# Performance work log

Measured on AMD Instinct MI355X. Metric: run time of the kernel, lower is better.

The kernel has to match this reference:

```python
import jax, jax.numpy as jnp
import numpy as np
import math

# irreps_in1 = 256x0e + 128x1e (dim 640); irreps_in2 = 1x0e + 1x1e (dim 4)
# TP/gate-input irreps = 256x0e + 128x0e + 128x1e (dim 768)
# gate output irreps   = 256x0e + 128x1e (dim 640)
MUL_S, MUL_V = 256, 128
DIM_IN1, DIM_IN2 = MUL_S + 3 * MUL_V, 4
FAN_IN = DIM_IN1 * DIM_IN2
N = 100000

# e3nn normalize2mom constants: 1/sqrt(E[f(x)^2]), x~N(0,1), via Gauss-Hermite
def _second_moment(f):
    t, w = np.polynomial.hermite.hermgauss(200)
    x = np.sqrt(2.0) * t
    return float(np.sum(w * f(x) ** 2) / np.sqrt(np.pi))

SILU_C = 1.0 / math.sqrt(_second_moment(lambda x: x / (1.0 + np.exp(-x))))
SIG_C = 1.0 / math.sqrt(_second_moment(lambda x: 1.0 / (1.0 + np.exp(-x))))

# e3nn path coefficients: sqrt(dim(ir_out) * path_weight / sum_paths_into_out) * w3j scale
# sum_paths (uvw, element norm) = sum(mul1*mul2) over instructions with same i_out
_XS01 = 256 + 128   # paths into each scalar output block
_XS2 = 256 + 128 + 128  # paths into vector output block
C0 = math.sqrt(1 * (256 * 256 * 1) / _XS01)                   # 0e x 0e -> 256x0e
C1 = math.sqrt(1 * (256 * 128 * 1) / _XS01) / math.sqrt(3.0)  # 1e x 1e -> 256x0e
C2 = math.sqrt(1 * (128 * 256 * 1) / _XS01)                   # 0e x 0e -> 128x0e
C3 = math.sqrt(1 * (128 * 128 * 1) / _XS01) / math.sqrt(3.0)  # 1e x 1e -> 128x0e
C4 = math.sqrt(3 * (128 * 256 * 1) / _XS2) / math.sqrt(3.0)   # 0e x 1e -> 128x1e
C5 = math.sqrt(3 * (128 * 128 * 1) / _XS2) / math.sqrt(3.0)   # 1e x 0e -> 128x1e
C6 = math.sqrt(3 * (128 * 128 * 1) / _XS2) / math.sqrt(6.0)   # 1e x 1e -> 128x1e (cross)


def setup_inputs() -> dict:
    key = jax.random.key(0)
    ks = jax.random.split(key, 10)
    return {
        'x': jax.random.normal(ks[0], (N, DIM_IN1), jnp.float32),
        'y': jax.random.normal(ks[1], (N, DIM_IN2), jnp.float32),
        'W0': jax.random.normal(ks[2], (256, 256), jnp.float32),
        'W1': jax.random.normal(ks[3], (128, 256), jnp.float32),
        'W2': jax.random.normal(ks[4], (256, 128), jnp.float32),
        'W3': jax.random.normal(ks[5], (128, 128), jnp.float32),
        'W4': jax.random.normal(ks[6], (256, 128), jnp.float32),
        'W5': jax.random.normal(ks[7], (128, 128), jnp.float32),
        'W6': jax.random.normal(ks[8], (128, 128), jnp.float32),
        'b': jax.random.normal(ks[9], (384,), jnp.float32) * 0.02,
    }


def reference(x, y, W0, W1, W2, W3, W4, W5, W6, b):
    n = x.shape[0]
    x0 = x[:, :MUL_S]                               # [N,256] scalars
    x1 = x[:, MUL_S:].reshape(n, MUL_V, 3)          # [N,128,3] vectors
    y0 = y[:, 0]                                    # [N]
    y1 = y[:, 1:]                                   # [N,3]

    x0y0 = x0 * y0[:, None]                         # [N,256]
    dot = jnp.einsum('zui,zi->zu', x1, y1)          # [N,128] (1e x 1e -> 0e)

    s1 = C0 * (x0y0 @ W0) + C1 * (dot @ W1)         # [N,256] scalar block
    s2 = C2 * (x0y0 @ W2) + C3 * (dot @ W3)         # [N,128] gate block

    va = C4 * (x0 @ W4)[:, :, None] * y1[:, None, :]            # 0e x 1e -> 1e
    vb = C5 * jnp.einsum('zui,uw->zwi', x1, W5) * y0[:, None, None]  # 1e x 0e -> 1e
    cross = jnp.cross(x1, y1[:, None, :])                        # [N,128,3]
    vc = C6 * jnp.einsum('zui,uw->zwi', cross, W6)               # 1e x 1e -> 1e
    v = va + vb + vc                                 # [N,128,3]

    inv = 1.0 / math.sqrt(FAN_IN)                    # rescale by sqrt(fan_in)
    s1 = s1 * inv + b[:MUL_S]
    s2 = s2 * inv + b[MUL_S:]
    v = v * inv

    out_s = SILU_C * jax.nn.silu(s1)                 # [N,256]
    gates = SIG_C * jax.nn.sigmoid(s2)               # [N,128]
    out_v = v * gates[:, :, None]                    # [N,128,3]
    return jnp.concatenate([out_s, out_v.reshape(n, -1)], axis=1)  # [N,640]
```

## Files before the change

kernel.cpp:

```cpp
#include <hip/hip_runtime.h>
#include <cmath>


typedef __bf16 bf16_t;
typedef bf16_t bf16x8 __attribute__((ext_vector_type(8)));
typedef bf16_t bf16x4 __attribute__((ext_vector_type(4)));
typedef float  f32x4  __attribute__((ext_vector_type(4)));

#define BM 32
#define KP 768

#define WU0 0
#define WD1 65536
#define WU2 98304
#define WD3 131072
#define WU4 147456
#define WR  180224
#define WQ  196608
#define WTOT 212992

#define MFMA(acc, av, bv) acc = __builtin_amdgcn_mfma_f32_16x16x32_bf16(av, bv, acc, 0, 0, 0)

__global__ void prep_weights(const float* __restrict__ W0, const float* __restrict__ W1,
                             const float* __restrict__ W2, const float* __restrict__ W3,
                             const float* __restrict__ W4, const float* __restrict__ W5,
                             const float* __restrict__ W6, bf16_t* __restrict__ WT,
                             float c0, float c1, float c2, float c3,
                             float c4, float c5, float c6)
{
    int idx = blockIdx.x * 256 + threadIdx.x;
    if (idx >= WTOT) return;
    float v;
    if (idx < WD1)      { int c = idx >> 8, k = idx & 255;                    v = c0 * W0[k * 256 + c]; }
    else if (idx < WU2) { int j = idx - WD1; int c = j >> 7, k = j & 127;     v = c1 * W1[k * 256 + c]; }
    else if (idx < WD3) { int j = idx - WU2; int c = j >> 8, k = j & 255;     v = c2 * W2[k * 128 + c]; }
    else if (idx < WU4) { int j = idx - WD3; int c = j >> 7, k = j & 127;     v = c3 * W3[k * 128 + c]; }
    else if (idx < WR)  { int j = idx - WU4; int c = j >> 8, k = j & 255;     v = c4 * W4[k * 128 + c]; }
    else if (idx < WQ)  { int j = idx - WR;  int c = j >> 7, k = j & 127;     v = c5 * W5[k * 128 + c]; }
    else                { int j = idx - WQ;  int c = j >> 7, k = j & 127;     v = c6 * W6[k * 128 + c]; }
    WT[idx] = (bf16_t)v;
}

__global__ __launch_bounds__(512) void tp_fused(
    const float* __restrict__ x, const float* __restrict__ y,
    const float* __restrict__ bias, const bf16_t* __restrict__ WT,
    float* __restrict__ out, float inv, float silu_c, float sig_c)
{
    __shared__ __attribute__((aligned(16))) bf16_t A[BM * KP];
    __shared__ float ylds[BM][4];

    const int tid = threadIdx.x;
    const int l   = tid & 63;
    const int w   = tid >> 6;
    const int l15 = l & 15;
    const int lg  = l >> 4;
    const int z0  = blockIdx.x * BM;

    if (tid < BM * 4) ylds[tid >> 2][tid & 3] = y[z0 * 4 + tid];

    #pragma unroll
    for (int it = 0; it < 4; ++it) {
        int f4 = tid + it * 512;
        int r = f4 >> 6, c4 = f4 & 63;
        float4 xv = *(const float4*)(x + (z0 + r) * 640 + c4 * 4);
        bf16x4 o;
        o[0] = (bf16_t)xv.x; o[1] = (bf16_t)xv.y; o[2] = (bf16_t)xv.z; o[3] = (bf16_t)xv.w;
        *(bf16x4*)&A[r * KP + ((c4 * 4) ^ ((r & 7) << 3))] = o;
    }
    #pragma unroll
    for (int it = 0; it < 8; ++it) {
        int e = tid + it * 512;
        int r = e >> 7, u = e & 127;
        const float* xp = x + (z0 + r) * 640 + 256 + u * 3;
        float a0 = xp[0], a1 = xp[1], a2 = xp[2];
        float4 yv = *(const float4*)(y + (z0 + r) * 4);
        int sw = (r & 7) << 3, base = r * KP;
        A[base + ((256 + u) ^ sw)] = (bf16_t)(a0 * yv.y + a1 * yv.z + a2 * yv.w);
        A[base + ((384 + u) ^ sw)] = (bf16_t)a0;
        A[base + ((512 + u) ^ sw)] = (bf16_t)a1;
        A[base + ((640 + u) ^ sw)] = (bf16_t)a2;
    }
    __syncthreads();

    const int asw    = (l15 & 7) << 3;
    const int a0base = l15 * KP;
    const int a1base = (16 + l15) * KP;
    const int klane  = lg * 8;

    {
        f32x4 sU[2][2], sD[2][2];
        #pragma unroll
        for (int a = 0; a < 2; ++a)
            #pragma unroll
            for (int b = 0; b < 2; ++b) { f32x4 z = {0.f,0.f,0.f,0.f}; sU[a][b] = z; sD[a][b] = z; }

        const bf16_t* b0p = WT + WU0 + ((w    ) * 16 + l15) * 256 + klane;
        const bf16_t* b1p = WT + WU0 + ((w + 8) * 16 + l15) * 256 + klane;
        const bf16_t* d0p = WT + WD1 + ((w    ) * 16 + l15) * 128 + klane;
        const bf16_t* d1p = WT + WD1 + ((w + 8) * 16 + l15) * 128 + klane;

        #pragma unroll
        for (int kk = 0; kk < 8; ++kk) {
            bf16x8 a0 = *(const bf16x8*)&A[a0base + ((kk * 32 + klane) ^ asw)];
            bf16x8 a1 = *(const bf16x8*)&A[a1base + ((kk * 32 + klane) ^ asw)];
            bf16x8 bb = *(const bf16x8*)(b0p + kk * 32);
            MFMA(sU[0][0], a0, bb); MFMA(sU[0][1], a1, bb);
            bb = *(const bf16x8*)(b1p + kk * 32);
            MFMA(sU[1][0], a0, bb); MFMA(sU[1][1], a1, bb);
        }
        #pragma unroll
        for (int kk = 0; kk < 4; ++kk) {
            bf16x8 a0 = *(const bf16x8*)&A[a0base + ((256 + kk * 32 + klane) ^ asw)];
            bf16x8 a1 = *(const bf16x8*)&A[a1base + ((256 + kk * 32 + klane) ^ asw)];
            bf16x8 bb = *(const bf16x8*)(d0p + kk * 32);
            MFMA(sD[0][0], a0, bb); MFMA(sD[0][1], a1, bb);
            bb = *(const bf16x8*)(d1p + kk * 32);
            MFMA(sD[1][0], a0, bb); MFMA(sD[1][1], a1, bb);
        }
        #pragma unroll
        for (int cs = 0; cs < 2; ++cs) {
            int col = (w + 8 * cs) * 16 + l15;
            float bv = bias[col];
            #pragma unroll
            for (int rt = 0; rt < 2; ++rt)
                #pragma unroll
                for (int rg = 0; rg < 4; ++rg) {
                    int lr = rt * 16 + lg * 4 + rg;
                    float sv = (ylds[lr][0] * sU[cs][rt][rg] + sD[cs][rt][rg]) * inv + bv;
                    out[(z0 + lr) * 640 + col] = silu_c * sv / (1.0f + __expf(-sv));
                }
        }
    }

    {
        f32x4 vU2[2], vU4[2], vD3[2], vR[3][2], vQ[3][2];
        #pragma unroll
        for (int rt = 0; rt < 2; ++rt) {
            f32x4 z = {0.f,0.f,0.f,0.f};
            vU2[rt] = z; vU4[rt] = z; vD3[rt] = z;
            #pragma unroll
            for (int i = 0; i < 3; ++i) { vR[i][rt] = z; vQ[i][rt] = z; }
        }
        const bf16_t* pu2 = WT + WU2 + (w * 16 + l15) * 256 + klane;
        const bf16_t* pu4 = WT + WU4 + (w * 16 + l15) * 256 + klane;
        const bf16_t* pd3 = WT + WD3 + (w * 16 + l15) * 128 + klane;
        const bf16_t* pr  = WT + WR  + (w * 16 + l15) * 128 + klane;
        const bf16_t* pq  = WT + WQ  + (w * 16 + l15) * 128 + klane;

        #pragma unroll
        for (int kk = 0; kk < 8; ++kk) {
            bf16x8 a0 = *(const bf16x8*)&A[a0base + ((kk * 32 + klane) ^ asw)];
            bf16x8 a1 = *(const bf16x8*)&A[a1base + ((kk * 32 + klane) ^ asw)];
            bf16x8 bb = *(const bf16x8*)(pu2 + kk * 32);
            MFMA(vU2[0], a0, bb); MFMA(vU2[1], a1, bb);
            bb = *(const bf16x8*)(pu4 + kk * 32);
            MFMA(vU4[0], a0, bb); MFMA(vU4[1], a1, bb);
        }
        #pragma unroll
        for (int kk = 0; kk < 4; ++kk) {
            bf16x8 a0 = *(const bf16x8*)&A[a0base + ((256 + kk * 32 + klane) ^ asw)];
            bf16x8 a1 = *(const bf16x8*)&A[a1base + ((256 + kk * 32 + klane) ^ asw)];
            bf16x8 bb = *(const bf16x8*)(pd3 + kk * 32);
            MFMA(vD3[0], a0, bb); MFMA(vD3[1], a1, bb);
        }
        #pragma unroll
        for (int kk = 0; kk < 4; ++kk) {
            bf16x8 brr = *(const bf16x8*)(pr + kk * 32);
            bf16x8 bqq = *(const bf16x8*)(pq + kk * 32);
            #pragma unroll
            for (int i = 0; i < 3; ++i) {
                int kb = 384 + i * 128 + kk * 32;
                bf16x8 a0 = *(const bf16x8*)&A[a0base + ((kb + klane) ^ asw)];
                bf16x8 a1 = *(const bf16x8*)&A[a1base + ((kb + klane) ^ asw)];
                MFMA(vR[i][0], a0, brr); MFMA(vR[i][1], a1, brr);
                MFMA(vQ[i][0], a0, bqq); MFMA(vQ[i][1], a1, bqq);
            }
        }

        int col = w * 16 + l15;
        float b2v = bias[256 + col];
        #pragma unroll
        for (int rt = 0; rt < 2; ++rt)
            #pragma unroll
            for (int rg = 0; rg < 4; ++rg) {
                int lr = rt * 16 + lg * 4 + rg;
                float y0 = ylds[lr][0], ya = ylds[lr][1], yb = ylds[lr][2], yc = ylds[lr][3];
                float sv = (y0 * vU2[rt][rg] + vD3[rt][rg]) * inv + b2v;
                float g  = sig_c * inv / (1.0f + __expf(-sv));
                float u4v = vU4[rt][rg];
                float v0 = ya * u4v + y0 * vR[0][rt][rg] + yc * vQ[1][rt][rg] - yb * vQ[2][rt][rg];
                float v1 = yb * u4v + y0 * vR[1][rt][rg] + ya * vQ[2][rt][rg] - yc * vQ[0][rt][rg];
                float v2 = yc * u4v + y0 * vR[2][rt][rg] + yb * vQ[0][rt][rg] - ya * vQ[1][rt][rg];
                int base = (z0 + lr) * 640 + 256 + col * 3;
                out[base + 0] = v0 * g;
                out[base + 1] = v1 * g;
                out[base + 2] = v2 * g;
            }
    }
}

extern "C" void kernel_launch(void* const* d_in, const int* in_sizes, int n_in,
                              void* d_out, int out_size, void* d_ws, size_t ws_size,
                              hipStream_t stream)
{
    (void)n_in; (void)out_size; (void)ws_size;
    const float* x  = (const float*)d_in[0];
    const float* y  = (const float*)d_in[1];
    const float* W0 = (const float*)d_in[2];
    const float* W1 = (const float*)d_in[3];
    const float* W2 = (const float*)d_in[4];
    const float* W3 = (const float*)d_in[5];
    const float* W4 = (const float*)d_in[6];
    const float* W5 = (const float*)d_in[7];
    const float* W6 = (const float*)d_in[8];
    const float* b  = (const float*)d_in[9];
    float* out = (float*)d_out;

    const int n = in_sizes[0] / 640;

    bf16_t* WT = (bf16_t*)d_ws;

    const double c0 = std::sqrt(256.0 * 256.0 / 384.0);
    const double c1 = std::sqrt(256.0 * 128.0 / 384.0) / std::sqrt(3.0);
    const double c2 = std::sqrt(128.0 * 256.0 / 384.0);
    const double c3 = std::sqrt(128.0 * 128.0 / 384.0) / std::sqrt(3.0);
    const double c4 = std::sqrt(3.0 * 128.0 * 256.0 / 512.0) / std::sqrt(3.0);
    const double c5 = std::sqrt(3.0 * 128.0 * 128.0 / 512.0) / std::sqrt(3.0);
    const double c6 = std::sqrt(3.0 * 128.0 * 128.0 / 512.0) / std::sqrt(6.0);
    const double inv = 1.0 / std::sqrt(2560.0);

    double m_silu = 0.0, m_sig = 0.0;
    {
        const int M = 24000;
        const double a = -12.0, h = 24.0 / M;
        for (int k = 0; k <= M; ++k) {
            double t = a + h * k;
            double wgt = (k == 0 || k == M) ? 1.0 : ((k & 1) ? 4.0 : 2.0);
            double sg = 1.0 / (1.0 + std::exp(-t));
            double phi = std::exp(-0.5 * t * t) * 0.3989422804014327;
            m_silu += wgt * (t * sg) * (t * sg) * phi;
            m_sig  += wgt * sg * sg * phi;
        }
        m_silu *= h / 3.0; m_sig *= h / 3.0;
    }
    const float silu_c = (float)(1.0 / std::sqrt(m_silu));
    const float sig_c  = (float)(1.0 / std::sqrt(m_sig));

    prep_weights<<<(WTOT + 255) / 256, 256, 0, stream>>>(
        W0, W1, W2, W3, W4, W5, W6, WT,
        (float)c0, (float)c1, (float)c2, (float)c3, (float)c4, (float)c5, (float)c6);

    tp_fused<<<n / BM, 512, 0, stream>>>(x, y, b, WT, out,
                                         (float)inv, silu_c, sig_c);
}
```

Baseline: 257.6 us.

## Make tp_fused persistent with double-buffered LDS and register-staged prefetch

Converts the kernel to a persistent grid of 256 blocks that loop over row tiles. The next tile's x/y values are prefetched into registers and written to a second LDS buffer while the current tile is computed, so global load latency can overlap with MFMA work. The vector-part staging now uses float4 loads and packed bf16x4 LDS writes, and the scalar and vector GEMM phases are merged into one pass over the A fragments. The costs are higher register pressure (many accumulators live at once, plus launch_bounds(512,2)), doubled LDS use, and a grid of 256 blocks that may underfill the GPU.

```diff
diff --git a/kernel.cpp b/kernel.cpp
--- a/kernel.cpp
+++ b/kernel.cpp
@@ -9,6 +9,7 @@
 
 #define BM 32
 #define KP 768
+#define NBLK 256
 
 #define WU0 0
 #define WD1 65536
@@ -41,82 +42,152 @@
     WT[idx] = (bf16_t)v;
 }
 
-__global__ __launch_bounds__(512) void tp_fused(
+__global__ __launch_bounds__(512, 2) void tp_fused(
     const float* __restrict__ x, const float* __restrict__ y,
     const float* __restrict__ bias, const bf16_t* __restrict__ WT,
-    float* __restrict__ out, float inv, float silu_c, float sig_c)
+    float* __restrict__ out, int NT, float inv, float silu_c, float sig_c)
 {
-    __shared__ __attribute__((aligned(16))) bf16_t A[BM * KP];
-    __shared__ float ylds[BM][4];
+    __shared__ __attribute__((aligned(16))) bf16_t Abuf[2][BM * KP];
+    __shared__ float Ybuf[2][BM][4];
 
     const int tid = threadIdx.x;
     const int l   = tid & 63;
     const int w   = tid >> 6;
     const int l15 = l & 15;
     const int lg  = l >> 4;
-    const int z0  = blockIdx.x * BM;
-
-    if (tid < BM * 4) ylds[tid >> 2][tid & 3] = y[z0 * 4 + tid];
-
-    #pragma unroll
-    for (int it = 0; it < 4; ++it) {
-        int f4 = tid + it * 512;
-        int r = f4 >> 6, c4 = f4 & 63;
-        float4 xv = *(const float4*)(x + (z0 + r) * 640 + c4 * 4);
-        bf16x4 o;
-        o[0] = (bf16_t)xv.x; o[1] = (bf16_t)xv.y; o[2] = (bf16_t)xv.z; o[3] = (bf16_t)xv.w;
-        *(bf16x4*)&A[r * KP + ((c4 * 4) ^ ((r & 7) << 3))] = o;
-    }
-    #pragma unroll
-    for (int it = 0; it < 8; ++it) {
-        int e = tid + it * 512;
-        int r = e >> 7, u = e & 127;
-        const float* xp = x + (z0 + r) * 640 + 256 + u * 3;
-        float a0 = xp[0], a1 = xp[1], a2 = xp[2];
-        float4 yv = *(const float4*)(y + (z0 + r) * 4);
-        int sw = (r & 7) << 3, base = r * KP;
-        A[base + ((256 + u) ^ sw)] = (bf16_t)(a0 * yv.y + a1 * yv.z + a2 * yv.w);
-        A[base + ((384 + u) ^ sw)] = (bf16_t)a0;
-        A[base + ((512 + u) ^ sw)] = (bf16_t)a1;
-        A[base + ((640 + u) ^ sw)] = (bf16_t)a2;
-    }
-    __syncthreads();
-
-    const int asw    = (l15 & 7) << 3;
+    const int klane = lg * 8;
+    const int asw   = (l15 & 7) << 3;
     const int a0base = l15 * KP;
     const int a1base = (16 + l15) * KP;
-    const int klane  = lg * 8;
-
-    {
-        f32x4 sU[2][2], sD[2][2];
-        #pragma unroll
-        for (int a = 0; a < 2; ++a)
-            #pragma unroll
-            for (int b = 0; b < 2; ++b) { f32x4 z = {0.f,0.f,0.f,0.f}; sU[a][b] = z; sD[a][b] = z; }
-
-        const bf16_t* b0p = WT + WU0 + ((w    ) * 16 + l15) * 256 + klane;
-        const bf16_t* b1p = WT + WU0 + ((w + 8) * 16 + l15) * 256 + klane;
-        const bf16_t* d0p = WT + WD1 + ((w    ) * 16 + l15) * 128 + klane;
-        const bf16_t* d1p = WT + WD1 + ((w + 8) * 16 + l15) * 128 + klane;
+    const int r0q = tid >> 5;
+    const int uq  = (tid & 31) * 4;
+
+    const bf16_t* b0p = WT + WU0 + ((w    ) * 16 + l15) * 256 + klane;
+    const bf16_t* b1p = WT + WU0 + ((w + 8) * 16 + l15) * 256 + klane;
+    const bf16_t* d0p = WT + WD1 + ((w    ) * 16 + l15) * 128 + klane;
+    const bf16_t* d1p = WT + WD1 + ((w + 8) * 16 + l15) * 128 + klane;
+    const bf16_t* pu2 = WT + WU2 + (w * 16 + l15) * 256 + klane;
+    const bf16_t* pd3 = WT + WD3 + (w * 16 + l15) * 128 + klane;
+    const bf16_t* pu4 = WT + WU4 + (w * 16 + l15) * 256 + klane;
+    const bf16_t* pr  = WT + WR  + (w * 16 + l15) * 128 + klane;
+    const bf16_t* pq  = WT + WQ  + (w * 16 + l15) * 128 + klane;
+
+    const int NTL = (NT - (int)blockIdx.x + NBLK - 1) / NBLK;
+    if (NTL <= 0) return;
+
+    float4 sx0[4], sx1[6], sy0, sy1, ybc;
+
+    auto STAGE = [&](int t) {
+        const float* xb = x + (size_t)t * (BM * 640);
+        #pragma unroll
+        for (int it = 0; it < 4; ++it) {
+            int f4 = tid + it * 512; int r = f4 >> 6, c4 = f4 & 63;
+            sx0[it] = *(const float4*)(xb + r * 640 + c4 * 4);
+        }
+        #pragma unroll
+        for (int s = 0; s < 2; ++s) {
+            int r = r0q + s * 16;
+            const float* xp = xb + r * 640 + 256 + (tid & 31) * 12;
+            sx1[s*3+0] = *(const float4*)(xp);
+            sx1[s*3+1] = *(const float4*)(xp + 4);
+            sx1[s*3+2] = *(const float4*)(xp + 8);
+        }
+        const float* yb = y + (size_t)t * (BM * 4);
+        sy0 = *(const float4*)(yb + r0q * 4);
+        sy1 = *(const float4*)(yb + (r0q + 16) * 4);
+        if (tid < 32) ybc = *(const float4*)(yb + tid * 4);
+    };
+
+    auto WRITE = [&](int p) {
+        if (tid < 32) *(float4*)&Ybuf[p][tid][0] = ybc;
+        #pragma unroll
+        for (int it = 0; it < 4; ++it) {
+            int f4 = tid + it * 512; int r = f4 >> 6, c4 = f4 & 63;
+            bf16x4 o;
+            o[0] = (bf16_t)sx0[it].x; o[1] = (bf16_t)sx0[it].y;
+            o[2] = (bf16_t)sx0[it].z; o[3] = (bf16_t)sx0[it].w;
+            *(bf16x4*)&Abuf[p][r * KP + ((c4 * 4) ^ ((r & 7) << 3))] = o;
+        }
+        #pragma unroll
+        for (int s = 0; s < 2; ++s) {
+            int r = r0q + s * 16;
+            int sw = (r & 7) << 3, base = r * KP;
+            float4 A0 = sx1[s*3+0], A1 = sx1[s*3+1], A2 = sx1[s*3+2];
+            float4 yv = s ? sy1 : sy0;
+            bf16x4 dq, e0, e1, e2;
+            dq[0] = (bf16_t)(A0.x*yv.y + A0.y*yv.z + A0.z*yv.w);
+            dq[1] = (bf16_t)(A0.w*yv.y + A1.x*yv.z + A1.y*yv.w);
+            dq[2] = (bf16_t)(A1.z*yv.y + A1.w*yv.z + A2.x*yv.w);
+            dq[3] = (bf16_t)(A2.y*yv.y + A2.z*yv.z + A2.w*yv.w);
+            e0[0]=(bf16_t)A0.x; e0[1]=(bf16_t)A0.w; e0[2]=(bf16_t)A1.z; e0[3]=(bf16_t)A2.y;
+            e1[0]=(bf16_t)A0.y; e1[1]=(bf16_t)A1.x; e1[2]=(bf16_t)A1.w; e1[3]=(bf16_t)A2.z;
+            e2[0]=(bf16_t)A0.z; e2[1]=(bf16_t)A1.y; e2[2]=(bf16_t)A2.x; e2[3]=(bf16_t)A2.w;
+            *(bf16x4*)&Abuf[p][base + ((256 + uq) ^ sw)] = dq;
+            *(bf16x4*)&Abuf[p][base + ((384 + uq) ^ sw)] = e0;
+            *(bf16x4*)&Abuf[p][base + ((512 + uq) ^ sw)] = e1;
+            *(bf16x4*)&Abuf[p][base + ((640 + uq) ^ sw)] = e2;
+        }
+    };
+
+    STAGE(blockIdx.x);
+    WRITE(0);
+    if (NTL > 1) STAGE(blockIdx.x + NBLK);
+
+    for (int j = 0; j < NTL; ++j) {
+        __syncthreads();
+        const int t = (int)blockIdx.x + j * NBLK;
+        const int p = j & 1;
+        const bf16_t* Ab = Abuf[p];
+
+        f32x4 sU[2][2], sD[2][2], vU2[2], vD3[2], vU4[2], vR[3][2], vQ[3][2];
+        {
+            f32x4 z = {0.f, 0.f, 0.f, 0.f};
+            #pragma unroll
+            for (int a = 0; a < 2; ++a)
+                #pragma unroll
+                for (int b = 0; b < 2; ++b) { sU[a][b] = z; sD[a][b] = z; }
+            #pragma unroll
+            for (int a = 0; a < 2; ++a) { vU2[a] = z; vD3[a] = z; vU4[a] = z; }
+            #pragma unroll
+            for (int i = 0; i < 3; ++i)
+                #pragma unroll
+                for (int a = 0; a < 2; ++a) { vR[i][a] = z; vQ[i][a] = z; }
+        }
 
         #pragma unroll
         for (int kk = 0; kk < 8; ++kk) {
-            bf16x8 a0 = *(const bf16x8*)&A[a0base + ((kk * 32 + klane) ^ asw)];
-            bf16x8 a1 = *(const bf16x8*)&A[a1base + ((kk * 32 + klane) ^ asw)];
-            bf16x8 bb = *(const bf16x8*)(b0p + kk * 32);
-            MFMA(sU[0][0], a0, bb); MFMA(sU[0][1], a1, bb);
-            bb = *(const bf16x8*)(b1p + kk * 32);
-            MFMA(sU[1][0], a0, bb); MFMA(sU[1][1], a1, bb);
+            bf16x8 a0 = *(const bf16x8*)&Ab[a0base + ((kk * 32 + klane) ^ asw)];
+            bf16x8 a1 = *(const bf16x8*)&Ab[a1base + ((kk * 32 + klane) ^ asw)];
+            bf16x8 bb;
+            bb = *(const bf16x8*)(b0p + kk * 32); MFMA(sU[0][0], a0, bb); MFMA(sU[0][1], a1, bb);
+            bb = *(const bf16x8*)(b1p + kk * 32); MFMA(sU[1][0], a0, bb); MFMA(sU[1][1], a1, bb);
+            bb = *(const bf16x8*)(pu2 + kk * 32); MFMA(vU2[0], a0, bb); MFMA(vU2[1], a1, bb);
+            bb = *(const bf16x8*)(pu4 + kk * 32); MFMA(vU4[0], a0, bb); MFMA(vU4[1], a1, bb);
         }
         #pragma unroll
         for (int kk = 0; kk < 4; ++kk) {
-            bf16x8 a0 = *(const bf16x8*)&A[a0base + ((256 + kk * 32 + klane) ^ asw)];
-            bf16x8 a1 = *(const bf16x8*)&A[a1base + ((256 + kk * 32 + klane) ^ asw)];
-            bf16x8 bb = *(const bf16x8*)(d0p + kk * 32);
-            MFMA(sD[0][0], a0, bb); MFMA(sD[0][1], a1, bb);
-            bb = *(const bf16x8*)(d1p + kk * 32);
-            MFMA(sD[1][0], a0, bb); MFMA(sD[1][1], a1, bb);
-        }
+            bf16x8 a0 = *(const bf16x8*)&Ab[a0base + ((256 + kk * 32 + klane) ^ asw)];
+            bf16x8 a1 = *(const bf16x8*)&Ab[a1base + ((256 + kk * 32 + klane) ^ asw)];
+            bf16x8 bb;
+            bb = *(const bf16x8*)(d0p + kk * 32); MFMA(sD[0][0], a0, bb); MFMA(sD[0][1], a1, bb);
+            bb = *(const bf16x8*)(d1p + kk * 32); MFMA(sD[1][0], a0, bb); MFMA(sD[1][1], a1, bb);
+            bb = *(const bf16x8*)(pd3 + kk * 32); MFMA(vD3[0], a0, bb); MFMA(vD3[1], a1, bb);
+        }
+        #pragma unroll
+        for (int kk = 0; kk < 4; ++kk) {
+            bf16x8 brr = *(const bf16x8*)(pr + kk * 32);
+            bf16x8 bqq = *(const bf16x8*)(pq + kk * 32);
+            #pragma unroll
+            for (int i = 0; i < 3; ++i) {
+                int kb = 384 + i * 128 + kk * 32;
+                bf16x8 a0 = *(const bf16x8*)&Ab[a0base + ((kb + klane) ^ asw)];
+                bf16x8 a1 = *(const bf16x8*)&Ab[a1base + ((kb + klane) ^ asw)];
+                MFMA(vR[i][0], a0, brr); MFMA(vR[i][1], a1, brr);
+                MFMA(vQ[i][0], a0, bqq); MFMA(vQ[i][1], a1, bqq);
+            }
+        }
+
+        const int rowb = t * BM;
         #pragma unroll
         for (int cs = 0; cs < 2; ++cs) {
             int col = (w + 8 * cs) * 16 + l15;
@@ -126,76 +197,34 @@
                 #pragma unroll
                 for (int rg = 0; rg < 4; ++rg) {
                     int lr = rt * 16 + lg * 4 + rg;
-                    float sv = (ylds[lr][0] * sU[cs][rt][rg] + sD[cs][rt][rg]) * inv + bv;
-                    out[(z0 + lr) * 640 + col] = silu_c * sv / (1.0f + __expf(-sv));
+                    float sv = (Ybuf[p][lr][0] * sU[cs][rt][rg] + sD[cs][rt][rg]) * inv + bv;
+                    out[(size_t)(rowb + lr) * 640 + col] = silu_c * sv / (1.0f + __expf(-sv));
                 }
         }
-    }
-
-    {
-        f32x4 vU2[2], vU4[2], vD3[2], vR[3][2], vQ[3][2];
-        #pragma unroll
-        for (int rt = 0; rt < 2; ++rt) {
-            f32x4 z = {0.f,0.f,0.f,0.f};
-            vU2[rt] = z; vU4[rt] = z; vD3[rt] = z;
-            #pragma unroll
-            for (int i = 0; i < 3; ++i) { vR[i][rt] = z; vQ[i][rt] = z; }
-        }
-        const bf16_t* pu2 = WT + WU2 + (w * 16 + l15) * 256 + klane;
-        const bf16_t* pu4 = WT + WU4 + (w * 16 + l15) * 256 + klane;
-        const bf16_t* pd3 = WT + WD3 + (w * 16 + l15) * 128 + klane;
-        const bf16_t* pr  = WT + WR  + (w * 16 + l15) * 128 + klane;
-        const bf16_t* pq  = WT + WQ  + (w * 16 + l15) * 128 + klane;
-
-        #pragma unroll
-        for (int kk = 0; kk < 8; ++kk) {
-            bf16x8 a0 = *(const bf16x8*)&A[a0base + ((kk * 32 + klane) ^ asw)];
-            bf16x8 a1 = *(const bf16x8*)&A[a1base + ((kk * 32 + klane) ^ asw)];
-            bf16x8 bb = *(const bf16x8*)(pu2 + kk * 32);
-            MFMA(vU2[0], a0, bb); MFMA(vU2[1], a1, bb);
-            bb = *(const bf16x8*)(pu4 + kk * 32);
-            MFMA(vU4[0], a0, bb); MFMA(vU4[1], a1, bb);
-        }
-        #pragma unroll
-        for (int kk = 0; kk < 4; ++kk) {
-            bf16x8 a0 = *(const bf16x8*)&A[a0base + ((256 + kk * 32 + klane) ^ asw)];
-            bf16x8 a1 = *(const bf16x8*)&A[a1base + ((256 + kk * 32 + klane) ^ asw)];
-            bf16x8 bb = *(const bf16x8*)(pd3 + kk * 32);
-            MFMA(vD3[0], a0, bb); MFMA(vD3[1], a1, bb);
-        }
-        #pragma unroll
-        for (int kk = 0; kk < 4; ++kk) {
-            bf16x8 brr = *(const bf16x8*)(pr + kk * 32);
-            bf16x8 bqq = *(const bf16x8*)(pq + kk * 32);
-            #pragma unroll
-            for (int i = 0; i < 3; ++i) {
-                int kb = 384 + i * 128 + kk * 32;
-                bf16x8 a0 = *(const bf16x8*)&A[a0base + ((kb + klane) ^ asw)];
-                bf16x8 a1 = *(const bf16x8*)&A[a1base + ((kb + klane) ^ asw)];
-                MFMA(vR[i][0], a0, brr); MFMA(vR[i][1], a1, brr);
-                MFMA(vQ[i][0], a0, bqq); MFMA(vQ[i][1], a1, bqq);
-            }
-        }
-
-        int col = w * 16 + l15;
-        float b2v = bias[256 + col];
-        #pragma unroll
-        for (int rt = 0; rt < 2; ++rt)
-            #pragma unroll
-            for (int rg = 0; rg < 4; ++rg) {
-                int lr = rt * 16 + lg * 4 + rg;
-                float y0 = ylds[lr][0], ya = ylds[lr][1], yb = ylds[lr][2], yc = ylds[lr][3];
-                float sv = (y0 * vU2[rt][rg] + vD3[rt][rg]) * inv + b2v;
-                float g  = sig_c * inv / (1.0f + __expf(-sv));
-                float u4v = vU4[rt][rg];
-                float v0 = ya * u4v + y0 * vR[0][rt][rg] + yc * vQ[1][rt][rg] - yb * vQ[2][rt][rg];
-                float v1 = yb * u4v + y0 * vR[1][rt][rg] + ya * vQ[2][rt][rg] - yc * vQ[0][rt][rg];
-                float v2 = yc * u4v + y0 * vR[2][rt][rg] + yb * vQ[0][rt][rg] - ya * vQ[1][rt][rg];
-                int base = (z0 + lr) * 640 + 256 + col * 3;
-                out[base + 0] = v0 * g;
-                out[base + 1] = v1 * g;
-                out[base + 2] = v2 * g;
-            }
+        {
+            int col = w * 16 + l15;
+            float b2v = bias[256 + col];
+            #pragma unroll
+            for (int rt = 0; rt < 2; ++rt)
+                #pragma unroll
+                for (int rg = 0; rg < 4; ++rg) {
+                    int lr = rt * 16 + lg * 4 + rg;
+                    float4 yv = *(const float4*)&Ybuf[p][lr][0];
+                    float sv = (yv.x * vU2[rt][rg] + vD3[rt][rg]) * inv + b2v;
+                    float g  = sig_c * inv / (1.0f + __expf(-sv));
+                    float u4v = vU4[rt][rg];
+                    float v0 = yv.y * u4v + yv.x * vR[0][rt][rg] + yv.w * vQ[1][rt][rg] - yv.z * vQ[2][rt][rg];
+                    float v1 = yv.z * u4v + yv.x * vR[1][rt][rg] + yv.y * vQ[2][rt][rg] - yv.w * vQ[0][rt][rg];
+                    float v2 = yv.w * u4v + yv.x * vR[2][rt][rg] + yv.z * vQ[0][rt][rg] - yv.y * vQ[1][rt][rg];
+                    size_t base = (size_t)(rowb + lr) * 640 + 256 + col * 3;
+                    out[base + 0] = v0 * g;
+                    out[base + 1] = v1 * g;
+                    out[base + 2] = v2 * g;
+                }
+        }
+
+        if (j + 1 < NTL) WRITE((j + 1) & 1);
+        if (j + 2 < NTL) STAGE((int)blockIdx.x + (j + 2) * NBLK);
     }
 }
 
@@ -216,7 +245,8 @@
     const float* b  = (const float*)d_in[9];
     float* out = (float*)d_out;
 
-    const int n = in_sizes[0] / 640;
+    const int n  = in_sizes[0] / 640;
+    const int NT = n / BM;
 
     bf16_t* WT = (bf16_t*)d_ws;
 
@@ -250,6 +280,7 @@
         W0, W1, W2, W3, W4, W5, W6, WT,
         (float)c0, (float)c1, (float)c2, (float)c3, (float)c4, (float)c5, (float)c6);
 
-    tp_fused<<<n / BM, 512, 0, stream>>>(x, y, b, WT, out,
-                                         (float)inv, silu_c, sig_c);
+    int grid = NT < NBLK ? NT : NBLK;
+    tp_fused<<<grid, 512, 0, stream>>>(x, y, b, WT, out, NT,
+                                       (float)inv, silu_c, sig_c);
 }
```

Result: slower. 604.8 us (+134.7%).

## Double row tile to 64 with 1024-thread blocks and vectorize vector-part staging

Applied to the files above, without the earlier changes.

Raises the block tile from 32 to 64 rows and the block size to 1024 threads. The 16 waves are split into 4 row groups by 4 column groups, so each wave now holds one row tile and several column tiles, which changes how weight fragments are reused from global memory. The vector-irrep staging now uses float4 loads of 12 contiguous floats per thread and bf16x4 LDS stores instead of scalar accesses. Bounds clamping and guarded stores are added for a tail when N is not a multiple of the tile. Shared memory doubles to about 96KB, which limits residency to one block per CU, and register pressure at 1024 threads may also rise.

```diff
diff --git a/kernel.cpp b/kernel.cpp
--- a/kernel.cpp
+++ b/kernel.cpp
@@ -7,7 +7,7 @@
 typedef bf16_t bf16x4 __attribute__((ext_vector_type(4)));
 typedef float  f32x4  __attribute__((ext_vector_type(4)));
 
-#define BM 32
+#define BM 64
 #define KP 768
 
 #define WU0 0
@@ -41,127 +41,142 @@
     WT[idx] = (bf16_t)v;
 }
 
-__global__ __launch_bounds__(512) void tp_fused(
+__global__ __launch_bounds__(1024) void tp_fused(
     const float* __restrict__ x, const float* __restrict__ y,
     const float* __restrict__ bias, const bf16_t* __restrict__ WT,
-    float* __restrict__ out, float inv, float silu_c, float sig_c)
+    float* __restrict__ out, int n, float inv, float silu_c, float sig_c)
 {
     __shared__ __attribute__((aligned(16))) bf16_t A[BM * KP];
-    __shared__ float ylds[BM][4];
+    __shared__ float Ylds[BM][4];
 
     const int tid = threadIdx.x;
     const int l   = tid & 63;
     const int w   = tid >> 6;
+    const int rg  = w >> 2;
+    const int cw  = w & 3;
     const int l15 = l & 15;
     const int lg  = l >> 4;
+    const int klane = lg * 8;
     const int z0  = blockIdx.x * BM;
 
-    if (tid < BM * 4) ylds[tid >> 2][tid & 3] = y[z0 * 4 + tid];
+    if (tid < BM * 4) {
+        int r = tid >> 2, c = tid & 3;
+        int zr = z0 + r; if (zr >= n) zr = n - 1;
+        Ylds[r][c] = y[(size_t)zr * 4 + c];
+    }
 
     #pragma unroll
     for (int it = 0; it < 4; ++it) {
-        int f4 = tid + it * 512;
+        int f4 = tid + it * 1024;
         int r = f4 >> 6, c4 = f4 & 63;
-        float4 xv = *(const float4*)(x + (z0 + r) * 640 + c4 * 4);
+        int zr = z0 + r; if (zr >= n) zr = n - 1;
+        float4 xv = *(const float4*)(x + (size_t)zr * 640 + c4 * 4);
         bf16x4 o;
-        o[0] = (bf16_t)xv.x; o[1] = (bf16_t)xv.y; o[2] = (bf16_t)xv.z; o[3] = (bf16_t)xv.w;
+        o[0] = (bf16_t)xv.x; o[1] = (bf16_t)xv.y;
+        o[2] = (bf16_t)xv.z; o[3] = (bf16_t)xv.w;
         *(bf16x4*)&A[r * KP + ((c4 * 4) ^ ((r & 7) << 3))] = o;
     }
     #pragma unroll
-    for (int it = 0; it < 8; ++it) {
-        int e = tid + it * 512;
-        int r = e >> 7, u = e & 127;
-        const float* xp = x + (z0 + r) * 640 + 256 + u * 3;
-        float a0 = xp[0], a1 = xp[1], a2 = xp[2];
-        float4 yv = *(const float4*)(y + (z0 + r) * 4);
+    for (int s = 0; s < 2; ++s) {
+        int r = (tid >> 5) + s * 32;
+        int zr = z0 + r; if (zr >= n) zr = n - 1;
+        const float* xp = x + (size_t)zr * 640 + 256 + (tid & 31) * 12;
+        float4 A0 = *(const float4*)(xp);
+        float4 A1 = *(const float4*)(xp + 4);
+        float4 A2 = *(const float4*)(xp + 8);
+        float4 yv = *(const float4*)(y + (size_t)zr * 4);
         int sw = (r & 7) << 3, base = r * KP;
-        A[base + ((256 + u) ^ sw)] = (bf16_t)(a0 * yv.y + a1 * yv.z + a2 * yv.w);
-        A[base + ((384 + u) ^ sw)] = (bf16_t)a0;
-        A[base + ((512 + u) ^ sw)] = (bf16_t)a1;
-        A[base + ((640 + u) ^ sw)] = (bf16_t)a2;
+        int uq = (tid & 31) * 4;
+        bf16x4 dq, e0, e1, e2;
+        dq[0] = (bf16_t)(A0.x*yv.y + A0.y*yv.z + A0.z*yv.w);
+        dq[1] = (bf16_t)(A0.w*yv.y + A1.x*yv.z + A1.y*yv.w);
+        dq[2] = (bf16_t)(A1.z*yv.y + A1.w*yv.z + A2.x*yv.w);
+        dq[3] = (bf16_t)(A2.y*yv.y + A2.z*yv.z + A2.w*yv.w);
+        e0[0]=(bf16_t)A0.x; e0[1]=(bf16_t)A0.w; e0[2]=(bf16_t)A1.z; e0[3]=(bf16_t)A2.y;
+        e1[0]=(bf16_t)A0.y; e1[1]=(bf16_t)A1.x; e1[2]=(bf16_t)A1.w; e1[3]=(bf16_t)A2.z;
+        e2[0]=(bf16_t)A0.z; e2[1]=(bf16_t)A1.y; e2[2]=(bf16_t)A2.x; e2[3]=(bf16_t)A2.w;
+        *(bf16x4*)&A[base + ((256 + uq) ^ sw)] = dq;
+        *(bf16x4*)&A[base + ((384 + uq) ^ sw)] = e0;
+        *(bf16x4*)&A[base + ((512 + uq) ^ sw)] = e1;
+        *(bf16x4*)&A[base + ((640 + uq) ^ sw)] = e2;
     }
     __syncthreads();
 
     const int asw    = (l15 & 7) << 3;
-    const int a0base = l15 * KP;
-    const int a1base = (16 + l15) * KP;
-    const int klane  = lg * 8;
+    const int a0base = (rg * 16 + l15) * KP;
 
     {
-        f32x4 sU[2][2], sD[2][2];
-        #pragma unroll
-        for (int a = 0; a < 2; ++a)
-            #pragma unroll
-            for (int b = 0; b < 2; ++b) { f32x4 z = {0.f,0.f,0.f,0.f}; sU[a][b] = z; sD[a][b] = z; }
-
-        const bf16_t* b0p = WT + WU0 + ((w    ) * 16 + l15) * 256 + klane;
-        const bf16_t* b1p = WT + WU0 + ((w + 8) * 16 + l15) * 256 + klane;
-        const bf16_t* d0p = WT + WD1 + ((w    ) * 16 + l15) * 128 + klane;
-        const bf16_t* d1p = WT + WD1 + ((w + 8) * 16 + l15) * 128 + klane;
+        const bf16_t* bS[4]; const bf16_t* bD[4];
+        #pragma unroll
+        for (int t = 0; t < 4; ++t) {
+            int ct = cw + 4 * t;
+            bS[t] = WT + WU0 + (ct * 16 + l15) * 256 + klane;
+            bD[t] = WT + WD1 + (ct * 16 + l15) * 128 + klane;
+        }
+        f32x4 sU[4], sD4[4];
+        #pragma unroll
+        for (int t = 0; t < 4; ++t) { f32x4 z = {0.f,0.f,0.f,0.f}; sU[t] = z; sD4[t] = z; }
 
         #pragma unroll
         for (int kk = 0; kk < 8; ++kk) {
             bf16x8 a0 = *(const bf16x8*)&A[a0base + ((kk * 32 + klane) ^ asw)];
-            bf16x8 a1 = *(const bf16x8*)&A[a1base + ((kk * 32 + klane) ^ asw)];
-            bf16x8 bb = *(const bf16x8*)(b0p + kk * 32);
-            MFMA(sU[0][0], a0, bb); MFMA(sU[0][1], a1, bb);
-            bb = *(const bf16x8*)(b1p + kk * 32);
-            MFMA(sU[1][0], a0, bb); MFMA(sU[1][1], a1, bb);
+            #pragma unroll
+            for (int t = 0; t < 4; ++t) {
+                bf16x8 bb = *(const bf16x8*)(bS[t] + kk * 32);
+                MFMA(sU[t], a0, bb);
+            }
         }
         #pragma unroll
         for (int kk = 0; kk < 4; ++kk) {
             bf16x8 a0 = *(const bf16x8*)&A[a0base + ((256 + kk * 32 + klane) ^ asw)];
-            bf16x8 a1 = *(const bf16x8*)&A[a1base + ((256 + kk * 32 + klane) ^ asw)];
-            bf16x8 bb = *(const bf16x8*)(d0p + kk * 32);
-            MFMA(sD[0][0], a0, bb); MFMA(sD[0][1], a1, bb);
-            bb = *(const bf16x8*)(d1p + kk * 32);
-            MFMA(sD[1][0], a0, bb); MFMA(sD[1][1], a1, bb);
-        }
-        #pragma unroll
-        for (int cs = 0; cs < 2; ++cs) {
-            int col = (w + 8 * cs) * 16 + l15;
+            #pragma unroll
+            for (int t = 0; t < 4; ++t) {
+                bf16x8 bb = *(const bf16x8*)(bD[t] + kk * 32);
+                MFMA(sD4[t], a0, bb);
+            }
+        }
+        #pragma unroll
+        for (int t = 0; t < 4; ++t) {
+            int col = (cw + 4 * t) * 16 + l15;
             float bv = bias[col];
             #pragma unroll
-            for (int rt = 0; rt < 2; ++rt)
-                #pragma unroll
-                for (int rg = 0; rg < 4; ++rg) {
-                    int lr = rt * 16 + lg * 4 + rg;
-                    float sv = (ylds[lr][0] * sU[cs][rt][rg] + sD[cs][rt][rg]) * inv + bv;
-                    out[(z0 + lr) * 640 + col] = silu_c * sv / (1.0f + __expf(-sv));
+            for (int reg = 0; reg < 4; ++reg) {
+                int lr = rg * 16 + lg * 4 + reg;
+                int zr = z0 + lr;
+                if (zr < n) {
+                    float sv = (Ylds[lr][0] * sU[t][reg] + sD4[t][reg]) * inv + bv;
+                    out[(size_t)zr * 640 + col] = silu_c * sv / (1.0f + __expf(-sv));
                 }
-        }
-    }
-
-    {
-        f32x4 vU2[2], vU4[2], vD3[2], vR[3][2], vQ[3][2];
-        #pragma unroll
-        for (int rt = 0; rt < 2; ++rt) {
-            f32x4 z = {0.f,0.f,0.f,0.f};
-            vU2[rt] = z; vU4[rt] = z; vD3[rt] = z;
-            #pragma unroll
-            for (int i = 0; i < 3; ++i) { vR[i][rt] = z; vQ[i][rt] = z; }
-        }
-        const bf16_t* pu2 = WT + WU2 + (w * 16 + l15) * 256 + klane;
-        const bf16_t* pu4 = WT + WU4 + (w * 16 + l15) * 256 + klane;
-        const bf16_t* pd3 = WT + WD3 + (w * 16 + l15) * 128 + klane;
-        const bf16_t* pr  = WT + WR  + (w * 16 + l15) * 128 + klane;
-        const bf16_t* pq  = WT + WQ  + (w * 16 + l15) * 128 + klane;
+            }
+        }
+    }
+
+    #pragma unroll
+    for (int t2 = 0; t2 < 2; ++t2) {
+        int ct = cw + 4 * t2;
+        const bf16_t* pu2 = WT + WU2 + (ct * 16 + l15) * 256 + klane;
+        const bf16_t* pd3 = WT + WD3 + (ct * 16 + l15) * 128 + klane;
+        const bf16_t* pu4 = WT + WU4 + (ct * 16 + l15) * 256 + klane;
+        const bf16_t* pr  = WT + WR  + (ct * 16 + l15) * 128 + klane;
+        const bf16_t* pq  = WT + WQ  + (ct * 16 + l15) * 128 + klane;
+
+        f32x4 vU2, vD3, vU4, vR[3], vQ[3];
+        { f32x4 z = {0.f,0.f,0.f,0.f}; vU2 = z; vD3 = z; vU4 = z;
+          #pragma unroll
+          for (int i = 0; i < 3; ++i) { vR[i] = z; vQ[i] = z; } }
 
         #pragma unroll
         for (int kk = 0; kk < 8; ++kk) {
             bf16x8 a0 = *(const bf16x8*)&A[a0base + ((kk * 32 + klane) ^ asw)];
-            bf16x8 a1 = *(const bf16x8*)&A[a1base + ((kk * 32 + klane) ^ asw)];
-            bf16x8 bb = *(const bf16x8*)(pu2 + kk * 32);
-            MFMA(vU2[0], a0, bb); MFMA(vU2[1], a1, bb);
-            bb = *(const bf16x8*)(pu4 + kk * 32);
-            MFMA(vU4[0], a0, bb); MFMA(vU4[1], a1, bb);
+            bf16x8 bb;
+            bb = *(const bf16x8*)(pu2 + kk * 32); MFMA(vU2, a0, bb);
+            bb = *(const bf16x8*)(pu4 + kk * 32); MFMA(vU4, a0, bb);
         }
         #pragma unroll
         for (int kk = 0; kk < 4; ++kk) {
             bf16x8 a0 = *(const bf16x8*)&A[a0base + ((256 + kk * 32 + klane) ^ asw)];
-            bf16x8 a1 = *(const bf16x8*)&A[a1base + ((256 + kk * 32 + klane) ^ asw)];
             bf16x8 bb = *(const bf16x8*)(pd3 + kk * 32);
-            MFMA(vD3[0], a0, bb); MFMA(vD3[1], a1, bb);
+            MFMA(vD3, a0, bb);
         }
         #pragma unroll
         for (int kk = 0; kk < 4; ++kk) {
@@ -171,31 +186,31 @@
             for (int i = 0; i < 3; ++i) {
                 int kb = 384 + i * 128 + kk * 32;
                 bf16x8 a0 = *(const bf16x8*)&A[a0base + ((kb + klane) ^ asw)];
-                bf16x8 a1 = *(const bf16x8*)&A[a1base + ((kb + klane) ^ asw)];
-                MFMA(vR[i][0], a0, brr); MFMA(vR[i][1], a1, brr);
-                MFMA(vQ[i][0], a0, bqq); MFMA(vQ[i][1], a1, bqq);
-            }
-        }
-
-        int col = w * 16 + l15;
+                MFMA(vR[i], a0, brr);
+                MFMA(vQ[i], a0, bqq);
+            }
+        }
+
+        int col = ct * 16 + l15;
         float b2v = bias[256 + col];
         #pragma unroll
-        for (int rt = 0; rt < 2; ++rt)
-            #pragma unroll
-            for (int rg = 0; rg < 4; ++rg) {
-                int lr = rt * 16 + lg * 4 + rg;
-                float y0 = ylds[lr][0], ya = ylds[lr][1], yb = ylds[lr][2], yc = ylds[lr][3];
-                float sv = (y0 * vU2[rt][rg] + vD3[rt][rg]) * inv + b2v;
+        for (int reg = 0; reg < 4; ++reg) {
+            int lr = rg * 16 + lg * 4 + reg;
+            int zr = z0 + lr;
+            if (zr < n) {
+                f32x4 yv = *(const f32x4*)&Ylds[lr][0];
+                float sv = (yv[0] * vU2[reg] + vD3[reg]) * inv + b2v;
                 float g  = sig_c * inv / (1.0f + __expf(-sv));
-                float u4v = vU4[rt][rg];
-                float v0 = ya * u4v + y0 * vR[0][rt][rg] + yc * vQ[1][rt][rg] - yb * vQ[2][rt][rg];
-                float v1 = yb * u4v + y0 * vR[1][rt][rg] + ya * vQ[2][rt][rg] - yc * vQ[0][rt][rg];
-                float v2 = yc * u4v + y0 * vR[2][rt][rg] + yb * vQ[0][rt][rg] - ya * vQ[1][rt][rg];
-                int base = (z0 + lr) * 640 + 256 + col * 3;
+                float u4v = vU4[reg];
+                float v0 = yv[1] * u4v + yv[0] * vR[0][reg] + yv[3] * vQ[1][reg] - yv[2] * vQ[2][reg];
+                float v1 = yv[2] * u4v + yv[0] * vR[1][reg] + yv[1] * vQ[2][reg] - yv[3] * vQ[0][reg];
+                float v2 = yv[3] * u4v + yv[0] * vR[2][reg] + yv[2] * vQ[0][reg] - yv[1] * vQ[1][reg];
+                size_t base = (size_t)zr * 640 + 256 + (size_t)col * 3;
                 out[base + 0] = v0 * g;
                 out[base + 1] = v1 * g;
                 out[base + 2] = v2 * g;
             }
+        }
     }
 }
 
@@ -250,6 +265,7 @@
         W0, W1, W2, W3, W4, W5, W6, WT,
         (float)c0, (float)c1, (float)c2, (float)c3, (float)c4, (float)c5, (float)c6);
 
-    tp_fused<<<n / BM, 512, 0, stream>>>(x, y, b, WT, out,
-                                         (float)inv, silu_c, sig_c);
+    const int grid = (n + BM - 1) / BM;
+    tp_fused<<<grid, 1024, 0, stream>>>(x, y, b, WT, out, n,
+                                        (float)inv, silu_c, sig_c);
 }
```

Result: slower. 438.8 us (+70.3%).
